# Optimization experiments

Hardware: AMD Instinct MI355X
Metric: run time of the kernel (lower is better)

The kernel has to match this reference:

```python
import jax, jax.numpy as jnp
import numpy as np

V, E, H = 10000, 256, 512
B, S = 8, 512


def setup_inputs() -> dict:
    key = jax.random.key(0)
    ks = jax.random.split(key, 6)
    return {
        "tokens": jax.random.randint(ks[0], (B, S), 0, V),
        "embed": jax.random.normal(ks[1], (V, E), dtype=jnp.float32) * 0.02,
        "w_ih": jax.random.normal(ks[2], (E, 4 * H), dtype=jnp.float32) * (1.0 / np.sqrt(E)),
        "w_hh": jax.random.normal(ks[3], (H, 4 * H), dtype=jnp.float32) * (1.0 / np.sqrt(H)),
        "bias": jnp.zeros((4 * H,), dtype=jnp.float32),
        "w_out": jax.random.normal(ks[4], (H, V), dtype=jnp.float32) * (1.0 / np.sqrt(H)),
        "b_out": jnp.zeros((V,), dtype=jnp.float32),
    }


def reference(tokens, embed, w_ih, w_hh, bias, w_out, b_out):
    bsz, seq = tokens.shape
    hid = w_hh.shape[0]
    x = embed[tokens]  # [B,S,E] embedding gather

    def step(carry, x_t):
        h, c = carry
        gates = x_t @ w_ih + h @ w_hh + bias  # [B,4H]
        i_t, f_t, g_t, o_t = jnp.split(gates, 4, axis=1)
        c = jax.nn.sigmoid(f_t) * c + jax.nn.sigmoid(i_t) * jnp.tanh(g_t)
        h = jax.nn.sigmoid(o_t) * jnp.tanh(c)
        return (h, c), h

    h0 = jnp.zeros((bsz, hid), dtype=x.dtype)  # zeros init broadcasts same as [H] zeros
    c0 = jnp.zeros((bsz, hid), dtype=x.dtype)
    (h_T, c_T), hs = jax.lax.scan(step, (h0, c0), jnp.swapaxes(x, 0, 1))
    hs = jnp.swapaxes(hs, 0, 1)  # [B,S,H]

    out = jax.nn.relu(hs @ w_out + b_out)  # [B,S,V]
    # nn.LogSoftmax() with no dim on a 3D tensor defaults to dim=0 (torch legacy
    # behavior); replicate faithfully.
    out = jax.nn.log_softmax(out, axis=0)
    return out, (h_T, c_T)
```

## Files before the change

### kernel.cpp

```cpp
#include <hip/hip_runtime.h>
#include <math.h>

#define V_  10000
#define E_  256
#define H_  512
#define B_  8
#define S_  512
#define G4H 2048
#define NPAD 10112

typedef __attribute__((ext_vector_type(8))) short bf16x8;
typedef __attribute__((ext_vector_type(4))) float f32x4;

__device__ __forceinline__ float sigmoidf_(float x) { return 1.f / (1.f + expf(-x)); }
__device__ __forceinline__ unsigned short f2bf(float x) {
  unsigned u = __float_as_uint(x);
  return (unsigned short)((u + 0x7fffu + ((u >> 16) & 1u)) >> 16);
}
__device__ __forceinline__ float bf2f(unsigned short h) {
  return __uint_as_float(((unsigned)h) << 16);
}

#define GLOAD_LDS16(gsrc, ldst)                                                       \
  __builtin_amdgcn_global_load_lds((const __attribute__((address_space(1))) unsigned*)(gsrc), \
                                   (__attribute__((address_space(3))) unsigned*)(ldst), 16, 0, 0)

__global__ __launch_bounds__(256, 4) void k_pre(
    const int* __restrict__ tokens, const float* __restrict__ embed,
    const float* __restrict__ w_ih, const float* __restrict__ bias,
    float* __restrict__ pre)
{
  __shared__ float A_lds[64 * 36];
  __shared__ float B_lds[32 * 64];
  __shared__ int   tok_lds[64];
  const int t  = threadIdx.x;
  const int m0 = blockIdx.x * 64;
  const int j0 = blockIdx.y * 64;
  if (t < 64) {
    int m = m0 + t;
    int s = m >> 3, b = m & 7;
    tok_lds[t] = tokens[b * S_ + s];
  }
  __syncthreads();
  const int tx = t & 15, ty = t >> 4;
  const int r_st = t >> 2, q_st = t & 3;
  const int kk_st = t >> 3, q2_st = t & 7;
  float acc[4][4] = {};
  for (int kt = 0; kt < E_; kt += 32) {
    {
      int tok = tok_lds[r_st];
      const float4* src = (const float4*)(embed + (size_t)tok * E_ + kt);
      float4 v0 = src[q_st];
      float4 v1 = src[q_st + 4];
      *(float4*)&A_lds[r_st * 36 + q_st * 4]       = v0;
      *(float4*)&A_lds[r_st * 36 + (q_st + 4) * 4] = v1;
    }
    {
      const float4* src = (const float4*)(w_ih + (size_t)(kt + kk_st) * G4H + j0);
      float4 v0 = src[q2_st];
      float4 v1 = src[q2_st + 8];
      *(float4*)&B_lds[kk_st * 64 + q2_st * 4]       = v0;
      *(float4*)&B_lds[kk_st * 64 + (q2_st + 8) * 4] = v1;
    }
    __syncthreads();
#pragma unroll
    for (int kkg = 0; kkg < 8; ++kkg) {
      float a_[4][4], b_[4][4];
#pragma unroll
      for (int i = 0; i < 4; ++i) {
        float4 av = *(const float4*)&A_lds[(ty * 4 + i) * 36 + kkg * 4];
        a_[i][0] = av.x; a_[i][1] = av.y; a_[i][2] = av.z; a_[i][3] = av.w;
      }
#pragma unroll
      for (int dk = 0; dk < 4; ++dk) {
        float4 bv = *(const float4*)&B_lds[(kkg * 4 + dk) * 64 + tx * 4];
        b_[dk][0] = bv.x; b_[dk][1] = bv.y; b_[dk][2] = bv.z; b_[dk][3] = bv.w;
      }
#pragma unroll
      for (int i = 0; i < 4; ++i)
#pragma unroll
        for (int dk = 0; dk < 4; ++dk)
#pragma unroll
          for (int j = 0; j < 4; ++j)
            acc[i][j] += a_[i][dk] * b_[dk][j];
    }
    __syncthreads();
  }
  const int j = j0 + tx * 4;
  float4 bi = *(const float4*)(bias + j);
#pragma unroll
  for (int i = 0; i < 4; ++i) {
    int m = m0 + ty * 4 + i;
    float4 o;
    o.x = acc[i][0] + bi.x; o.y = acc[i][1] + bi.y;
    o.z = acc[i][2] + bi.z; o.w = acc[i][3] + bi.w;
    *(float4*)&pre[(size_t)m * G4H + j] = o;
  }
}

__global__ __launch_bounds__(256, 4) void k_wconv(
    const float* __restrict__ w_out,
    unsigned short* __restrict__ wT_hi, unsigned short* __restrict__ wT_lo)
{
  __shared__ float tile[64][65];
  const int t  = threadIdx.x;
  const int n0 = blockIdx.x * 64;
  const int k0 = blockIdx.y * 64;
  const int cn = (t & 15) * 4, rk = t >> 4;
#pragma unroll
  for (int p = 0; p < 4; ++p) {
    int k = k0 + rk + p * 16;
    int n = n0 + cn;
    float v[4];
    if (n + 3 < V_) {
      float4 x = *(const float4*)(w_out + (size_t)k * V_ + n);
      v[0] = x.x; v[1] = x.y; v[2] = x.z; v[3] = x.w;
    } else {
#pragma unroll
      for (int j = 0; j < 4; ++j) v[j] = (n + j < V_) ? w_out[(size_t)k * V_ + n + j] : 0.f;
    }
#pragma unroll
    for (int j = 0; j < 4; ++j) tile[rk + p * 16][cn + j] = v[j];
  }
  __syncthreads();
  const int n_l = t >> 2, kq = t & 3;
  unsigned short hib[16], lob[16];
#pragma unroll
  for (int j = 0; j < 16; ++j) {
    float x = tile[kq * 16 + j][n_l];
    unsigned short h = f2bf(x);
    hib[j] = h;
    lob[j] = f2bf(x - bf2f(h));
  }
  size_t base = (size_t)(n0 + n_l) * 512 + k0 + kq * 16;
#pragma unroll
  for (int q = 0; q < 4; ++q) {
    *(ushort4*)&wT_hi[base + q * 4] = *(ushort4*)&hib[q * 4];
    *(ushort4*)&wT_lo[base + q * 4] = *(ushort4*)&lob[q * 4];
  }
}

__global__ __launch_bounds__(512, 2) void k_rec(
    const float* __restrict__ pre, const float* __restrict__ w_hh,
    unsigned long long* __restrict__ hbuf,
    unsigned short* __restrict__ hs_hi,
    unsigned short* __restrict__ hs_lo,
    float* __restrict__ out_tail)
{
  __shared__ float h_lds[H_];
  __shared__ float partials[16 * 32 * 4];
  __shared__ float gates_lds[32 * 4];

  const int t   = threadIdx.x;
  const int bid = blockIdx.x;
  const int c   = bid >> 4;
  const int r   = bid & 15;
  const int u0  = r * 32;
  const int u_l = t & 31;
  const int kq  = t >> 5;
  const int k0  = kq * 32;
  const int ug  = u0 + u_l;

  float4 wreg[32];
#pragma unroll
  for (int i = 0; i < 32; ++i) {
    const float* wr = w_hh + (size_t)(k0 + i) * G4H + ug;
    wreg[i] = make_float4(wr[0], wr[512], wr[1024], wr[1536]);
  }

  const bool is_act = (t < 32);
  float c_state = 0.f;

  for (int s = 0; s < S_; ++s) {
    float p0 = 0.f, p1 = 0.f, p2 = 0.f, p3 = 0.f;
    if (is_act) {
      const float* pp = pre + ((size_t)(s * B_ + c)) * G4H + u0 + t;
      p0 = pp[0]; p1 = pp[512]; p2 = pp[1024]; p3 = pp[1536];
    }
    {
      const unsigned long long* src = hbuf + (((s & 1) * B_ + c) * H_) + t;
      unsigned long long v;
      do {
        v = __hip_atomic_load(src, __ATOMIC_RELAXED, __HIP_MEMORY_SCOPE_AGENT);
      } while ((unsigned)(v >> 32) != (unsigned)s);
      h_lds[t] = __uint_as_float((unsigned)v);
    }
    float a0 = 0.f, a1 = 0.f, a2 = 0.f, a3 = 0.f;
#pragma unroll
    for (int i = 0; i < 32; ++i) {
      float hv = h_lds[k0 + i];
      a0 += wreg[i].x * hv; a1 += wreg[i].y * hv;
      a2 += wreg[i].z * hv; a3 += wreg[i].w * hv;
    }
    *(float4*)&partials[t * 4] = make_float4(a0, a1, a2, a3);
    __syncthreads();
    if (t < 128) {
      const int uu = t >> 2, g = t & 3;
      float ssum = 0.f;
#pragma unroll
      for (int q = 0; q < 16; ++q) ssum += partials[(q * 32 + uu) * 4 + g];
      gates_lds[t] = ssum;
    }
    __syncthreads();
    if (is_act) {
      float gi = gates_lds[t * 4 + 0] + p0;
      float gf = gates_lds[t * 4 + 1] + p1;
      float gg = gates_lds[t * 4 + 2] + p2;
      float go = gates_lds[t * 4 + 3] + p3;
      float ig = sigmoidf_(gi), fg = sigmoidf_(gf);
      float gt = tanhf(gg),     og = sigmoidf_(go);
      c_state = fg * c_state + ig * gt;
      float h = og * tanhf(c_state);
      size_t hidx = ((size_t)(s * B_ + c)) * H_ + u0 + t;
      unsigned short hh = f2bf(h);
      hs_hi[hidx] = hh;
      hs_lo[hidx] = f2bf(h - bf2f(hh));
      unsigned long long pk =
          ((unsigned long long)(unsigned)(s + 1) << 32) | (unsigned long long)__float_as_uint(h);
      __hip_atomic_store(hbuf + ((((s + 1) & 1) * B_ + c) * H_) + u0 + t, pk,
                         __ATOMIC_RELAXED, __HIP_MEMORY_SCOPE_AGENT);
      if (s == S_ - 1) {
        out_tail[c * H_ + u0 + t]            = h;
        out_tail[B_ * H_ + c * H_ + u0 + t]  = c_state;
      }
    }
  }
}

__global__ __launch_bounds__(256, 2) void k_out(
    const unsigned short* __restrict__ hs_hi, const unsigned short* __restrict__ hs_lo,
    const unsigned short* __restrict__ wT_hi, const unsigned short* __restrict__ wT_lo,
    const float* __restrict__ b_out, float* __restrict__ out)
{
  __shared__ unsigned short lds[4 * 128 * 64];
  char* ldsc = (char*)lds;
  const int t  = threadIdx.x;
  const int w  = t >> 6, l = t & 63;
  const int m0 = blockIdx.x * 128;
  const int n0 = blockIdx.y * 128;
  const int wm = w >> 1, wn = w & 1;
  const int lm = l & 15, lq = l >> 4;

  f32x4 acc[4][4];
#pragma unroll
  for (int fm = 0; fm < 4; ++fm)
#pragma unroll
    for (int fn = 0; fn < 4; ++fn) acc[fm][fn] = (f32x4){0.f, 0.f, 0.f, 0.f};

  for (int kt = 0; kt < H_; kt += 64) {
#pragma unroll
    for (int i = 0; i < 4; ++i) {
      int o   = i * 4096 + w * 1024 + l * 16;
      int r   = o >> 7;
      int c16 = (o >> 4) & 7;
      int cs  = c16 ^ (r & 7);
      const unsigned short* sAh = hs_hi + (size_t)(m0 + r) * 512 + kt + cs * 8;
      const unsigned short* sAl = hs_lo + (size_t)(m0 + r) * 512 + kt + cs * 8;
      const unsigned short* sBh = wT_hi + (size_t)(n0 + r) * 512 + kt + cs * 8;
      const unsigned short* sBl = wT_lo + (size_t)(n0 + r) * 512 + kt + cs * 8;
      GLOAD_LDS16(sAh, ldsc + 0     + i * 4096 + w * 1024);
      GLOAD_LDS16(sAl, ldsc + 16384 + i * 4096 + w * 1024);
      GLOAD_LDS16(sBh, ldsc + 32768 + i * 4096 + w * 1024);
      GLOAD_LDS16(sBl, ldsc + 49152 + i * 4096 + w * 1024);
    }
    __syncthreads();
#pragma unroll
    for (int ks = 0; ks < 2; ++ks) {
      bf16x8 ah[4], al[4], bh[4], bl[4];
#pragma unroll
      for (int f = 0; f < 4; ++f) {
        int ra = wm * 64 + f * 16 + lm;
        int ca = (ks * 4 + lq) ^ (ra & 7);
        ah[f] = *(const bf16x8*)(ldsc + 0     + ra * 128 + ca * 16);
        al[f] = *(const bf16x8*)(ldsc + 16384 + ra * 128 + ca * 16);
        int rb = wn * 64 + f * 16 + lm;
        int cb = (ks * 4 + lq) ^ (rb & 7);
        bh[f] = *(const bf16x8*)(ldsc + 32768 + rb * 128 + cb * 16);
        bl[f] = *(const bf16x8*)(ldsc + 49152 + rb * 128 + cb * 16);
      }
#pragma unroll
      for (int fm = 0; fm < 4; ++fm)
#pragma unroll
        for (int fn = 0; fn < 4; ++fn) {
          acc[fm][fn] = __builtin_amdgcn_mfma_f32_16x16x32_bf16(ah[fm], bh[fn], acc[fm][fn], 0, 0, 0);
          acc[fm][fn] = __builtin_amdgcn_mfma_f32_16x16x32_bf16(ah[fm], bl[fn], acc[fm][fn], 0, 0, 0);
          acc[fm][fn] = __builtin_amdgcn_mfma_f32_16x16x32_bf16(al[fm], bh[fn], acc[fm][fn], 0, 0, 0);
        }
    }
    __syncthreads();
  }

#pragma unroll
  for (int fn = 0; fn < 4; ++fn) {
    const int n = n0 + wn * 64 + fn * 16 + lm;
    const float bo = (n < V_) ? b_out[n] : 0.f;
#pragma unroll
    for (int fm = 0; fm < 4; ++fm) {
      float v[4];
#pragma unroll
      for (int rg = 0; rg < 4; ++rg) v[rg] = fmaxf(acc[fm][fn][rg] + bo, 0.f);
      float mx = fmaxf(fmaxf(v[0], v[1]), fmaxf(v[2], v[3]));
      float gm = fmaxf(mx, __shfl_xor(mx, 16, 64));
      float ss = expf(v[0] - gm) + expf(v[1] - gm) + expf(v[2] - gm) + expf(v[3] - gm);
      float lse = gm + logf(ss + __shfl_xor(ss, 16, 64));
      if (n < V_) {
#pragma unroll
        for (int rg = 0; rg < 4; ++rg) {
          int m = m0 + wm * 64 + fm * 16 + lq * 4 + rg;
          int s = m >> 3, b = m & 7;
          out[(size_t)b * ((size_t)S_ * V_) + (size_t)s * V_ + n] = v[rg] - lse;
        }
      }
    }
  }
}

extern "C" void kernel_launch(void* const* d_in, const int* in_sizes, int n_in,
                              void* d_out, int out_size, void* d_ws, size_t ws_size,
                              hipStream_t stream) {
  const int*   tokens = (const int*)d_in[0];
  const float* embed  = (const float*)d_in[1];
  const float* w_ih   = (const float*)d_in[2];
  const float* w_hh   = (const float*)d_in[3];
  const float* bias   = (const float*)d_in[4];
  const float* w_out  = (const float*)d_in[5];
  const float* b_out  = (const float*)d_in[6];
  float* out = (float*)d_out;

  char* ws = (char*)d_ws;
  float*              pre   = (float*)(ws);
  unsigned short*     hs_hi = (unsigned short*)(ws + 33554432);
  unsigned short*     hs_lo = (unsigned short*)(ws + 37748736);
  unsigned short*     wT_hi = (unsigned short*)(ws + 41943040);
  unsigned short*     wT_lo = (unsigned short*)(ws + 52297728);
  unsigned long long* hbuf  = (unsigned long long*)(ws + 62652416);

  hipMemsetAsync(hbuf, 0, 2 * B_ * H_ * sizeof(unsigned long long), stream);

  k_wconv<<<dim3(158, 8), 256, 0, stream>>>(w_out, wT_hi, wT_lo);
  k_pre<<<dim3(64, 32), 256, 0, stream>>>(tokens, embed, w_ih, bias, pre);
  k_rec<<<dim3(128), 512, 0, stream>>>(pre, w_hh, hbuf, hs_hi, hs_lo,
                                       out + (size_t)B_ * S_ * V_);
  k_out<<<dim3(32, 79), 256, 0, stream>>>(hs_hi, hs_lo, wT_hi, wT_lo, b_out, out);
}
```

Measured before the change: 1.206 ms.

## Reduce LSTM recurrence partials with wave shuffles and use fast activations

The recurrent kernel now gives each wavefront 4 hidden units and splits the K dimension across lanes. Partial gate sums are combined with xor-shuffles inside the wave, which removes the LDS partials buffer and two of the three block barriers per timestep. The h vector is double-buffered in padded LDS and read as float4, and the next h is published before the bf16 hs stores. Sigmoid and tanh switch to clamped exp2/rcp approximations, which lowers the latency of the serial step at some cost in accuracy. The block-to-batch mapping also changes.

```diff
diff --git a/kernel.cpp b/kernel.cpp
--- a/kernel.cpp
+++ b/kernel.cpp
@@ -19,6 +19,15 @@
 }
 __device__ __forceinline__ float bf2f(unsigned short h) {
   return __uint_as_float(((unsigned)h) << 16);
+}
+__device__ __forceinline__ float fsig(float x) {
+  x = fminf(fmaxf(x, -30.f), 30.f);
+  return __builtin_amdgcn_rcpf(1.f + __builtin_amdgcn_exp2f(-1.44269504f * x));
+}
+__device__ __forceinline__ float ftanh(float x) {
+  x = fminf(fmaxf(x, -9.f), 9.f);
+  float E = __builtin_amdgcn_exp2f(2.88539008f * x);
+  return (E - 1.f) * __builtin_amdgcn_rcpf(E + 1.f);
 }
 
 #define GLOAD_LDS16(gsrc, ldst)                                                       \
@@ -147,81 +156,77 @@
     unsigned short* __restrict__ hs_lo,
     float* __restrict__ out_tail)
 {
-  __shared__ float h_lds[H_];
-  __shared__ float partials[16 * 32 * 4];
-  __shared__ float gates_lds[32 * 4];
-
-  const int t   = threadIdx.x;
-  const int bid = blockIdx.x;
-  const int c   = bid >> 4;
-  const int r   = bid & 15;
-  const int u0  = r * 32;
-  const int u_l = t & 31;
-  const int kq  = t >> 5;
-  const int k0  = kq * 32;
-  const int ug  = u0 + u_l;
+  __shared__ float4 h4_lds[2 * 144];
+  float* hf = (float*)h4_lds;
+  const int t  = threadIdx.x;
+  const int c  = blockIdx.x & 7;
+  const int r  = blockIdx.x >> 3;
+  const int u0 = r * 32;
+  const int w  = t >> 6, l = t & 63;
+  const int ul = l & 3, kq = l >> 2;
+  const int u  = u0 + w * 4 + ul;
+  const int pw = (t >> 5) * 36 + (t & 31);
 
   float4 wreg[32];
+  const int k0 = kq * 32;
 #pragma unroll
   for (int i = 0; i < 32; ++i) {
-    const float* wr = w_hh + (size_t)(k0 + i) * G4H + ug;
+    const float* wr = w_hh + (size_t)(k0 + i) * G4H + u;
     wreg[i] = make_float4(wr[0], wr[512], wr[1024], wr[1536]);
   }
-
-  const bool is_act = (t < 32);
+  const bool is_act = (kq == 0);
   float c_state = 0.f;
 
   for (int s = 0; s < S_; ++s) {
+    const int par = s & 1;
     float p0 = 0.f, p1 = 0.f, p2 = 0.f, p3 = 0.f;
     if (is_act) {
-      const float* pp = pre + ((size_t)(s * B_ + c)) * G4H + u0 + t;
+      const float* pp = pre + ((size_t)(s * B_ + c)) * G4H + u;
       p0 = pp[0]; p1 = pp[512]; p2 = pp[1024]; p3 = pp[1536];
     }
     {
-      const unsigned long long* src = hbuf + (((s & 1) * B_ + c) * H_) + t;
-      unsigned long long v;
-      do {
+      const unsigned long long* src = hbuf + ((par * B_ + c) * H_) + t;
+      unsigned long long v = __hip_atomic_load(src, __ATOMIC_RELAXED, __HIP_MEMORY_SCOPE_AGENT);
+      while ((unsigned)(v >> 32) != (unsigned)s)
         v = __hip_atomic_load(src, __ATOMIC_RELAXED, __HIP_MEMORY_SCOPE_AGENT);
-      } while ((unsigned)(v >> 32) != (unsigned)s);
-      h_lds[t] = __uint_as_float((unsigned)v);
-    }
+      hf[par * 576 + pw] = __uint_as_float((unsigned)v);
+    }
+    __syncthreads();
     float a0 = 0.f, a1 = 0.f, a2 = 0.f, a3 = 0.f;
-#pragma unroll
-    for (int i = 0; i < 32; ++i) {
-      float hv = h_lds[k0 + i];
-      a0 += wreg[i].x * hv; a1 += wreg[i].y * hv;
-      a2 += wreg[i].z * hv; a3 += wreg[i].w * hv;
-    }
-    *(float4*)&partials[t * 4] = make_float4(a0, a1, a2, a3);
-    __syncthreads();
-    if (t < 128) {
-      const int uu = t >> 2, g = t & 3;
-      float ssum = 0.f;
-#pragma unroll
-      for (int q = 0; q < 16; ++q) ssum += partials[(q * 32 + uu) * 4 + g];
-      gates_lds[t] = ssum;
-    }
-    __syncthreads();
+    const float4* h4 = h4_lds + par * 144 + kq * 9;
+#pragma unroll
+    for (int i4 = 0; i4 < 8; ++i4) {
+      float4 hv = h4[i4];
+      float4 w0 = wreg[i4 * 4 + 0], w1 = wreg[i4 * 4 + 1];
+      float4 w2 = wreg[i4 * 4 + 2], w3 = wreg[i4 * 4 + 3];
+      a0 += w0.x * hv.x + w1.x * hv.y + w2.x * hv.z + w3.x * hv.w;
+      a1 += w0.y * hv.x + w1.y * hv.y + w2.y * hv.z + w3.y * hv.w;
+      a2 += w0.z * hv.x + w1.z * hv.y + w2.z * hv.z + w3.z * hv.w;
+      a3 += w0.w * hv.x + w1.w * hv.y + w2.w * hv.z + w3.w * hv.w;
+    }
+#pragma unroll
+    for (int mask = 4; mask <= 32; mask <<= 1) {
+      a0 += __shfl_xor(a0, mask, 64);
+      a1 += __shfl_xor(a1, mask, 64);
+      a2 += __shfl_xor(a2, mask, 64);
+      a3 += __shfl_xor(a3, mask, 64);
+    }
     if (is_act) {
-      float gi = gates_lds[t * 4 + 0] + p0;
-      float gf = gates_lds[t * 4 + 1] + p1;
-      float gg = gates_lds[t * 4 + 2] + p2;
-      float go = gates_lds[t * 4 + 3] + p3;
-      float ig = sigmoidf_(gi), fg = sigmoidf_(gf);
-      float gt = tanhf(gg),     og = sigmoidf_(go);
+      float gi = a0 + p0, gf = a1 + p1, gg = a2 + p2, go = a3 + p3;
+      float ig = fsig(gi), fg = fsig(gf), gt = ftanh(gg), og = fsig(go);
       c_state = fg * c_state + ig * gt;
-      float h = og * tanhf(c_state);
-      size_t hidx = ((size_t)(s * B_ + c)) * H_ + u0 + t;
+      float h = og * ftanh(c_state);
+      unsigned long long pk = ((unsigned long long)(unsigned)(s + 1) << 32)
+                            | (unsigned long long)__float_as_uint(h);
+      __hip_atomic_store(hbuf + ((((s + 1) & 1) * B_ + c) * H_) + u, pk,
+                         __ATOMIC_RELAXED, __HIP_MEMORY_SCOPE_AGENT);
+      size_t hidx = ((size_t)(s * B_ + c)) * H_ + u;
       unsigned short hh = f2bf(h);
       hs_hi[hidx] = hh;
       hs_lo[hidx] = f2bf(h - bf2f(hh));
-      unsigned long long pk =
-          ((unsigned long long)(unsigned)(s + 1) << 32) | (unsigned long long)__float_as_uint(h);
-      __hip_atomic_store(hbuf + ((((s + 1) & 1) * B_ + c) * H_) + u0 + t, pk,
-                         __ATOMIC_RELAXED, __HIP_MEMORY_SCOPE_AGENT);
       if (s == S_ - 1) {
-        out_tail[c * H_ + u0 + t]            = h;
-        out_tail[B_ * H_ + c * H_ + u0 + t]  = c_state;
+        out_tail[c * H_ + u]           = h;
+        out_tail[B_ * H_ + c * H_ + u] = c_state;
       }
     }
   }
```

After: 1.733 ms. 43.7% more time.
